# Optimization experiments

Hardware: AMD Instinct MI355X
Metric: run time of the kernel (lower is better)

Reference implementation:

```python
import jax, jax.numpy as jnp
import numpy as np

N_HEADS = 16
EPS = 1e-4


def setup_inputs() -> dict:
    key = jax.random.key(0)
    ks = jax.random.split(key, 9)
    B, L, E = 4, 4096, 1024
    s = 1.0 / np.sqrt(E)
    return {
        "x": jax.random.normal(ks[0], (B, L, E), dtype=jnp.float32),
        "Wq": jax.random.normal(ks[1], (E, E), dtype=jnp.float32) * s,
        "bq": jax.random.normal(ks[2], (E,), dtype=jnp.float32) * 0.01,
        "Wk": jax.random.normal(ks[3], (E, E), dtype=jnp.float32) * s,
        "bk": jax.random.normal(ks[4], (E,), dtype=jnp.float32) * 0.01,
        "Wv": jax.random.normal(ks[5], (E, E), dtype=jnp.float32) * s,
        "bv": jax.random.normal(ks[6], (E,), dtype=jnp.float32) * 0.01,
        "Wo": jax.random.normal(ks[7], (E, E), dtype=jnp.float32) * s,
        "bo": jax.random.normal(ks[8], (E,), dtype=jnp.float32) * 0.01,
    }


def _cosformer(x, Wq, bq, Wk, bk, Wv, bv, Wo, bo):
    B, L, E = x.shape
    H = N_HEADS
    hd = E // H
    # torch Linear: y = x @ W.T + b; self-attention so q=k=v source is x
    q = jax.nn.relu(jnp.einsum('ble,fe->blf', x, Wq) + bq)
    k = jax.nn.relu(jnp.einsum('ble,fe->blf', x, Wk) + bk)
    v = jnp.einsum('ble,fe->blf', x, Wv) + bv
    # (B, L, E) -> (B*H, L, hd)  [matches torch view(L, B*H, hd).transpose(0,1)]
    def split_heads(t):
        return t.reshape(B, L, H, hd).transpose(0, 2, 1, 3).reshape(B * H, L, hd)
    q, k, v = split_heads(q), split_heads(k), split_heads(v)
    m = L  # src_len == tgt_len
    idx = (np.pi / 2) * jnp.arange(1, m + 1, dtype=jnp.float32) / m  # (m,)
    sin = jnp.sin(idx)[None, :, None]
    cos = jnp.cos(idx)[None, :, None]
    q_ = jnp.concatenate([q * sin, q * cos], axis=-1)  # (BH, L, 2hd)
    k_ = jnp.concatenate([k * sin, k * cos], axis=-1)
    kv = jnp.einsum('nld,nlm->ndm', k_, v)             # (BH, 2hd, hd)
    z = 1.0 / jnp.maximum(jnp.einsum('nld,nd->nl', q_, k_.sum(axis=1)), EPS)
    attn = jnp.einsum('nld,ndm->nlm', q_, kv) * z[:, :, None]  # (BH, L, hd)
    # (B*H, L, hd) -> (B, L, E)
    out = attn.reshape(B, H, L, hd).transpose(0, 2, 1, 3).reshape(B, L, E)
    return jnp.einsum('ble,fe->blf', out, Wo) + bo


def reference(x, Wq, bq, Wk, bk, Wv, bv, Wo, bo):
    return _cosformer(x, Wq, bq, Wk, bk, Wv, bv, Wo, bo)
```

## Files before the change

### kernel.cpp

```cpp
#include <hip/hip_runtime.h>


typedef unsigned short u16;
typedef unsigned int u32;
typedef __attribute__((ext_vector_type(8))) __bf16 bf16x8;
typedef __attribute__((ext_vector_type(4))) float f32x4;

#define PI_HALF 1.57079632679489662f
#define EPS_Z 1e-4f

__device__ __forceinline__ u16 f32_to_bf16(float f) {
    union { float f; unsigned int u; } x; x.f = f;
    unsigned int lsb = (x.u >> 16) & 1u;
    x.u += 0x7fffu + lsb;
    return (u16)(x.u >> 16);
}
__device__ __forceinline__ float bf16_to_f32(u16 u) {
    union { float f; unsigned int u; } x; x.u = ((unsigned int)u) << 16;
    return x.f;
}

typedef __attribute__((address_space(1))) void amdgpu_global_t;
typedef __attribute__((address_space(3))) void amdgpu_lds_t;
__device__ __forceinline__ void async_load16(const u16* g, u16* l) {
    __builtin_amdgcn_global_load_lds((amdgpu_global_t*)g, (amdgpu_lds_t*)l, 16, 0, 0);
}

__global__ __launch_bounds__(256) void cvt_bf16(const float* __restrict__ in,
                                                u16* __restrict__ out, int n4) {
    int i = blockIdx.x * 256 + threadIdx.x;
    if (i >= n4) return;
    float4 f = ((const float4*)in)[i];
    ushort4 o;
    o.x = f32_to_bf16(f.x); o.y = f32_to_bf16(f.y);
    o.z = f32_to_bf16(f.z); o.w = f32_to_bf16(f.w);
    ((ushort4*)out)[i] = o;
}

__global__ __launch_bounds__(256) void cvt_w4(const float* __restrict__ w0,
                                              const float* __restrict__ w1,
                                              const float* __restrict__ w2,
                                              const float* __restrict__ w3,
                                              u16* __restrict__ wcat) {
    const float* src = (blockIdx.y == 0) ? w0 : (blockIdx.y == 1) ? w1
                     : (blockIdx.y == 2) ? w2 : w3;
    u16* dst = wcat + (size_t)blockIdx.y * 1048576;
    int i = blockIdx.x * 256 + threadIdx.x;
    float4 f = ((const float4*)src)[i];
    ushort4 o;
    o.x = f32_to_bf16(f.x); o.y = f32_to_bf16(f.y);
    o.z = f32_to_bf16(f.z); o.w = f32_to_bf16(f.w);
    ((ushort4*)dst)[i] = o;
}

__global__ __launch_bounds__(256) void gemm_qkv(const u16* __restrict__ A,
                                                const u16* __restrict__ Wcat,
                                                const float* __restrict__ bq,
                                                const float* __restrict__ bk,
                                                const float* __restrict__ bv,
                                                u16* __restrict__ qo,
                                                u16* __restrict__ ko,
                                                u16* __restrict__ vo) {
    __shared__ u16 As[128 * 32];
    __shared__ u16 Bs[128 * 32];
    const int K = 1024;
    const int tid  = threadIdx.x;
    const int wave = tid >> 6;
    const int lane = tid & 63;
    const int quad = lane >> 4;
    const int l15  = lane & 15;
    const long tileM = (long)blockIdx.x * 128;
    const long tileN = (long)blockIdx.y * 128;
    const int mat = blockIdx.y >> 3;
    const float* bias = (mat == 0) ? bq : (mat == 1) ? bk : bv;
    u16* outp = (mat == 0) ? qo : (mat == 1) ? ko : vo;
    const bool relu = (mat < 2);
    const int wm = (wave >> 1) * 64;
    const int wn = (wave & 1) * 64;
    const int s_row = wave * 32 + (lane >> 2);
    const int s_col = (lane & 3) * 8;

    const u16* gA = A    + (tileM + s_row) * (long)K + s_col;
    const u16* gB = Wcat + (tileN + s_row) * (long)K + s_col;
    u16* lA = &As[wave * 1024];
    u16* lB = &Bs[wave * 1024];

    f32x4 acc[4][4] = {};

    for (int kb = 0; kb < K; kb += 32) {
        async_load16(gA,                lA);
        async_load16(gA + 16 * (long)K, lA + 512);
        async_load16(gB,                lB);
        async_load16(gB + 16 * (long)K, lB + 512);
        gA += 32; gB += 32;
        __syncthreads();
        bf16x8 af[4], bf[4];
#pragma unroll
        for (int i = 0; i < 4; i++) {
            af[i] = *(const bf16x8*)&As[(wm + i * 16 + l15) * 32 + quad * 8];
            bf[i] = *(const bf16x8*)&Bs[(wn + i * 16 + l15) * 32 + quad * 8];
        }
#pragma unroll
        for (int i = 0; i < 4; i++)
#pragma unroll
            for (int j = 0; j < 4; j++)
                acc[i][j] = __builtin_amdgcn_mfma_f32_16x16x32_bf16(
                    af[i], bf[j], acc[i][j], 0, 0, 0);
        __syncthreads();
    }

#pragma unroll
    for (int j = 0; j < 4; j++) {
        const long n = tileN + wn + j * 16 + l15;
        const int nl = (int)n & 1023;
        const float bv_ = bias[nl];
#pragma unroll
        for (int i = 0; i < 4; i++) {
            const long m0 = tileM + wm + i * 16 + quad * 4;
#pragma unroll
            for (int r = 0; r < 4; r++) {
                float v = acc[i][j][r] + bv_;
                if (relu) v = fmaxf(v, 0.0f);
                outp[(m0 + r) * 1024 + nl] = f32_to_bf16(v);
            }
        }
    }
}

__global__ __launch_bounds__(256) void gemm_o(const u16* __restrict__ A,
                                              const u16* __restrict__ Bw,
                                              const float* __restrict__ bias,
                                              float* __restrict__ Cout,
                                              int M, int N, int K) {
    __shared__ u16 As[128 * 32];
    __shared__ u16 Bs[128 * 32];
    const int tid  = threadIdx.x;
    const int wave = tid >> 6;
    const int lane = tid & 63;
    const int quad = lane >> 4;
    const int l15  = lane & 15;
    const long tileM = (long)blockIdx.x * 128;
    const long tileN = (long)blockIdx.y * 128;
    const int wm = (wave >> 1) * 64;
    const int wn = (wave & 1) * 64;
    const int s_row = wave * 32 + (lane >> 2);
    const int s_col = (lane & 3) * 8;

    const u16* gA = A  + (tileM + s_row) * (long)K + s_col;
    const u16* gB = Bw + (tileN + s_row) * (long)K + s_col;
    u16* lA = &As[wave * 1024];
    u16* lB = &Bs[wave * 1024];

    f32x4 acc[4][4] = {};

    for (int kb = 0; kb < K; kb += 32) {
        async_load16(gA,                lA);
        async_load16(gA + 16 * (long)K, lA + 512);
        async_load16(gB,                lB);
        async_load16(gB + 16 * (long)K, lB + 512);
        gA += 32; gB += 32;
        __syncthreads();
        bf16x8 af[4], bf[4];
#pragma unroll
        for (int i = 0; i < 4; i++) {
            af[i] = *(const bf16x8*)&As[(wm + i * 16 + l15) * 32 + quad * 8];
            bf[i] = *(const bf16x8*)&Bs[(wn + i * 16 + l15) * 32 + quad * 8];
        }
#pragma unroll
        for (int i = 0; i < 4; i++)
#pragma unroll
            for (int j = 0; j < 4; j++)
                acc[i][j] = __builtin_amdgcn_mfma_f32_16x16x32_bf16(
                    af[i], bf[j], acc[i][j], 0, 0, 0);
        __syncthreads();
    }

#pragma unroll
    for (int j = 0; j < 4; j++) {
        const long n = tileN + wn + j * 16 + l15;
        const float bv = bias[n];
#pragma unroll
        for (int i = 0; i < 4; i++) {
            const long m0 = tileM + wm + i * 16 + quad * 4;
#pragma unroll
            for (int r = 0; r < 4; r++)
                Cout[(m0 + r) * (long)N + n] = acc[i][j][r] + bv;
        }
    }
}

__global__ __launch_bounds__(256) void kv_mfma(const u16* __restrict__ kmat,
                                               const u16* __restrict__ vmat,
                                               float* __restrict__ part) {
    __shared__ u16 Ak[64 * 40];
    __shared__ u16 Bv[64 * 40];
    const int tid = threadIdx.x;
    const int wave = tid >> 6, lane = tid & 63;
    const int quad = lane >> 4, l15 = lane & 15;
    const int head = blockIdx.y;
    const int b = head >> 4, h = head & 15;
    const int l0 = blockIdx.x * 512;
    const int sl = tid >> 3;
    const int sc8 = tid & 7;
    const int scol = sl ^ ((sc8 & 3) << 3);
    const int krow_base = (wave & 1) * 32;
    const bool use_cos = (wave >> 1) != 0;
    const int mbase = wave * 32;

    float sv[8], cv[8];
#pragma unroll
    for (int e = 0; e < 8; e++) {
        float ang = (PI_HALF / 4096.0f) * (float)(l0 + quad * 8 + e + 1);
        sv[e] = sinf(ang); cv[e] = cosf(ang);
    }
    const float cD = 0.9999247018391445f;
    const float sD = 0.0122715382857199f;

    bf16x8 onesf;
#pragma unroll
    for (int e = 0; e < 8; e++)
        onesf[e] = (l15 == 0) ? (__bf16)1.0f : (__bf16)0.0f;

    f32x4 acc[2][5] = {};

    for (int kt = 0; kt < 16; kt++) {
        const long row = ((long)b * 4096 + l0 + kt * 32 + sl) * 1024 + h * 64 + sc8 * 8;
        uint4 kk = *(const uint4*)(kmat + row);
        uint4 vv = *(const uint4*)(vmat + row);
        const u16* kp = (const u16*)&kk;
        const u16* vp = (const u16*)&vv;
#pragma unroll
        for (int e = 0; e < 8; e++) {
            const int d = sc8 * 8 + e;
            Ak[d * 40 + scol] = kp[e];
            Bv[d * 40 + scol] = vp[e];
        }
        __syncthreads();

        bf16x8 af[2];
#pragma unroll
        for (int i = 0; i < 2; i++) {
            const int d = krow_base + i * 16 + l15;
            const int q2 = (quad ^ ((d >> 3) & 3)) * 8;
            bf16x8 raw = *(const bf16x8*)&Ak[d * 40 + q2];
            bf16x8 sc;
#pragma unroll
            for (int e = 0; e < 8; e++)
                sc[e] = (__bf16)((float)raw[e] * (use_cos ? cv[e] : sv[e]));
            af[i] = sc;
        }
        bf16x8 bfr[5];
#pragma unroll
        for (int j = 0; j < 4; j++) {
            const int n = j * 16 + l15;
            const int q2 = (quad ^ ((n >> 3) & 3)) * 8;
            bfr[j] = *(const bf16x8*)&Bv[n * 40 + q2];
        }
        bfr[4] = onesf;
#pragma unroll
        for (int i = 0; i < 2; i++)
#pragma unroll
            for (int j = 0; j < 5; j++)
                acc[i][j] = __builtin_amdgcn_mfma_f32_16x16x32_bf16(
                    af[i], bfr[j], acc[i][j], 0, 0, 0);

#pragma unroll
        for (int e = 0; e < 8; e++) {
            const float ns = sv[e] * cD + cv[e] * sD;
            cv[e] = cv[e] * cD - sv[e] * sD;
            sv[e] = ns;
        }
        __syncthreads();
    }

    float* op = part + ((long)blockIdx.x * 64 + head) * 10240;
#pragma unroll
    for (int i = 0; i < 2; i++)
#pragma unroll
        for (int j = 0; j < 5; j++)
#pragma unroll
            for (int r = 0; r < 4; r++)
                op[(mbase + i * 16 + quad * 4 + r) * 80 + j * 16 + l15] = acc[i][j][r];
}

__global__ __launch_bounds__(256) void kv_reduce_t(const float* __restrict__ part,
                                                   u16* __restrict__ Bt) {
    __shared__ float accs[32 * 81];
    const int head = blockIdx.y, d2t = blockIdx.x;
    const float* bp = part + (long)head * 10240 + d2t * 32 * 80;
    for (int idx = threadIdx.x; idx < 2560; idx += 256) {
        float s = 0.0f;
#pragma unroll
        for (int c = 0; c < 8; c++) s += bp[(long)c * 655360 + idx];
        const int d2 = idx / 80, n = idx - d2 * 80;
        accs[d2 * 81 + n] = s;
    }
    __syncthreads();
    for (int idx = threadIdx.x; idx < 2560; idx += 256) {
        const int n = idx >> 5, d2 = idx & 31;
        Bt[(long)head * 10240 + n * 128 + d2t * 32 + d2] = f32_to_bf16(accs[d2 * 81 + n]);
    }
}

__global__ __launch_bounds__(256) void attn_mfma(const u16* __restrict__ qb,
                                                 const u16* __restrict__ Bt,
                                                 u16* __restrict__ merged) {
    __shared__ __align__(16) u16 As[128 * 72];
    __shared__ __align__(16) u16 Bs[80 * 136];
    const int tid = threadIdx.x;
    const int wave = tid >> 6, lane = tid & 63;
    const int quad = lane >> 4, l15 = lane & 15;
    const int head = blockIdx.y;
    const int b = head >> 4, h = head & 15;
    const int tm = blockIdx.x * 128;
    const long b4 = (long)b * 4096;

    for (int c = tid; c < 1024; c += 256) {
        const int row = c >> 3, c8 = c & 7;
        uint4 t = *(const uint4*)(qb + (b4 + tm + row) * 1024 + h * 64 + c8 * 8);
        *(uint4*)&As[row * 72 + c8 * 8] = t;
    }
    for (int c = tid; c < 1280; c += 256) {
        const int row = c >> 4, c16 = c & 15;
        uint4 t = *(const uint4*)(Bt + (long)head * 10240 + row * 128 + c16 * 8);
        *(uint4*)&Bs[row * 136 + c16 * 8] = t;
    }
    const int wm = wave * 32;
    float snl[2], csl[2];
#pragma unroll
    for (int i = 0; i < 2; i++) {
        const int l = tm + wm + i * 16 + l15;
        const float idx = PI_HALF * (float)(l + 1) * (1.0f / 4096.0f);
        snl[i] = sinf(idx); csl[i] = cosf(idx);
    }
    __syncthreads();

    f32x4 acc[2][5] = {};
#pragma unroll
    for (int kb = 0; kb < 4; kb++) {
        const int qc = (kb & 1) * 32 + quad * 8;
        bf16x8 af[2];
#pragma unroll
        for (int i = 0; i < 2; i++) {
            bf16x8 raw = *(const bf16x8*)&As[(wm + i * 16 + l15) * 72 + qc];
            const float s = (kb < 2) ? snl[i] : csl[i];
            bf16x8 sc;
#pragma unroll
            for (int e = 0; e < 8; e++) sc[e] = (__bf16)((float)raw[e] * s);
            af[i] = sc;
        }
        bf16x8 bf[5];
#pragma unroll
        for (int j = 0; j < 5; j++)
            bf[j] = *(const bf16x8*)&Bs[(j * 16 + l15) * 136 + kb * 32 + quad * 8];
#pragma unroll
        for (int i = 0; i < 2; i++)
#pragma unroll
            for (int j = 0; j < 5; j++)
                acc[i][j] = __builtin_amdgcn_mfma_f32_16x16x32_bf16(
                    af[i], bf[j], acc[i][j], 0, 0, 0);
    }

#pragma unroll
    for (int i = 0; i < 2; i++) {
        float z[4];
#pragma unroll
        for (int r = 0; r < 4; r++) {
            const float den = __shfl(acc[i][4][r], lane & 0x30, 64);
            z[r] = 1.0f / fmaxf(den, EPS_Z);
        }
#pragma unroll
        for (int j = 0; j < 4; j++)
#pragma unroll
            for (int r = 0; r < 4; r++) {
                const int l = tm + wm + i * 16 + quad * 4 + r;
                merged[(b4 + l) * 1024 + h * 64 + j * 16 + l15] =
                    f32_to_bf16(acc[i][j][r] * z[r]);
            }
    }
}

extern "C" void kernel_launch(void* const* d_in, const int* in_sizes, int n_in,
                              void* d_out, int out_size, void* d_ws, size_t ws_size,
                              hipStream_t stream) {
    (void)in_sizes; (void)n_in; (void)out_size; (void)ws_size;
    const float* x  = (const float*)d_in[0];
    const float* Wq = (const float*)d_in[1];
    const float* bq = (const float*)d_in[2];
    const float* Wk = (const float*)d_in[3];
    const float* bk = (const float*)d_in[4];
    const float* Wv = (const float*)d_in[5];
    const float* bv = (const float*)d_in[6];
    const float* Wo = (const float*)d_in[7];
    const float* bo = (const float*)d_in[8];
    float* out = (float*)d_out;

    const int M = 16384, E = 1024;
    char* ws = (char*)d_ws;
    const size_t MB = 1048576;
    u16* xb   = (u16*)(ws);
    u16* qb   = (u16*)(ws + 32 * MB);
    u16* kb   = (u16*)(ws + 64 * MB);
    u16* vb   = (u16*)(ws + 96 * MB);
    u16* wcat = (u16*)(ws + 128 * MB);
    u16* wob  = wcat + 3 * (size_t)E * E;
    u16* Btb  = (u16*)(ws + 136 * MB);
    float* part = (float*)xb;
    u16* mergedb = kb;

    cvt_bf16<<<dim3(M * E / 4 / 256), dim3(256), 0, stream>>>(x, xb, M * E / 4);
    cvt_w4<<<dim3(E * E / 4 / 256, 4), dim3(256), 0, stream>>>(Wq, Wk, Wv, Wo, wcat);

    gemm_qkv<<<dim3(M / 128, 24), dim3(256), 0, stream>>>(xb, wcat, bq, bk, bv,
                                                          qb, kb, vb);

    kv_mfma<<<dim3(8, 64), dim3(256), 0, stream>>>(kb, vb, part);
    kv_reduce_t<<<dim3(4, 64), dim3(256), 0, stream>>>(part, Btb);
    attn_mfma<<<dim3(32, 64), dim3(256), 0, stream>>>(qb, Btb, mergedb);

    gemm_o<<<dim3(M / 128, E / 128), dim3(256), 0, stream>>>(mergedb, wob, bo,
                                                             out, M, E, E);
}
```

Baseline: 384.0 us.

## Write K and V transposed from QKV GEMM so kv_mfma reads fragments directly

```diff
diff --git a/kernel.cpp b/kernel.cpp
--- a/kernel.cpp
+++ b/kernel.cpp
@@ -59,8 +59,8 @@
                                                 const float* __restrict__ bk,
                                                 const float* __restrict__ bv,
                                                 u16* __restrict__ qo,
-                                                u16* __restrict__ ko,
-                                                u16* __restrict__ vo) {
+                                                u16* __restrict__ kTo,
+                                                u16* __restrict__ vTo) {
     __shared__ u16 As[128 * 32];
     __shared__ u16 Bs[128 * 32];
     const int K = 1024;
@@ -73,8 +73,6 @@
     const long tileN = (long)blockIdx.y * 128;
     const int mat = blockIdx.y >> 3;
     const float* bias = (mat == 0) ? bq : (mat == 1) ? bk : bv;
-    u16* outp = (mat == 0) ? qo : (mat == 1) ? ko : vo;
-    const bool relu = (mat < 2);
     const int wm = (wave >> 1) * 64;
     const int wn = (wave & 1) * 64;
     const int s_row = wave * 32 + (lane >> 2);
@@ -109,19 +107,43 @@
         __syncthreads();
     }
 
-#pragma unroll
-    for (int j = 0; j < 4; j++) {
-        const long n = tileN + wn + j * 16 + l15;
-        const int nl = (int)n & 1023;
-        const float bv_ = bias[nl];
-#pragma unroll
-        for (int i = 0; i < 4; i++) {
-            const long m0 = tileM + wm + i * 16 + quad * 4;
-#pragma unroll
-            for (int r = 0; r < 4; r++) {
-                float v = acc[i][j][r] + bv_;
-                if (relu) v = fmaxf(v, 0.0f);
-                outp[(m0 + r) * 1024 + nl] = f32_to_bf16(v);
+    if (mat == 0) {
+#pragma unroll
+        for (int j = 0; j < 4; j++) {
+            const int nl = (int)(tileN + wn + j * 16 + l15) & 1023;
+            const float bv_ = bias[nl];
+#pragma unroll
+            for (int i = 0; i < 4; i++) {
+                const long m0 = tileM + wm + i * 16 + quad * 4;
+#pragma unroll
+                for (int r = 0; r < 4; r++) {
+                    float v = fmaxf(acc[i][j][r] + bv_, 0.0f);
+                    qo[(m0 + r) * 1024 + nl] = f32_to_bf16(v);
+                }
+            }
+        }
+    } else {
+        u16* outT = (mat == 1) ? kTo : vTo;
+        const bool relu = (mat == 1);
+#pragma unroll
+        for (int j = 0; j < 4; j++) {
+            const int nl = (int)(tileN + wn + j * 16 + l15) & 1023;
+            const float bv_ = bias[nl];
+#pragma unroll
+            for (int i = 0; i < 4; i++) {
+                const long m0 = tileM + wm + i * 16 + quad * 4;
+                float v0 = acc[i][j][0] + bv_;
+                float v1 = acc[i][j][1] + bv_;
+                float v2 = acc[i][j][2] + bv_;
+                float v3 = acc[i][j][3] + bv_;
+                if (relu) {
+                    v0 = fmaxf(v0, 0.0f); v1 = fmaxf(v1, 0.0f);
+                    v2 = fmaxf(v2, 0.0f); v3 = fmaxf(v3, 0.0f);
+                }
+                u32 p0 = (u32)f32_to_bf16(v0) | ((u32)f32_to_bf16(v1) << 16);
+                u32 p1 = (u32)f32_to_bf16(v2) | ((u32)f32_to_bf16(v3) << 16);
+                u32* dst = (u32*)(outT + (size_t)nl * 16384 + m0);
+                dst[0] = p0; dst[1] = p1;
             }
         }
     }
@@ -189,28 +211,35 @@
     }
 }
 
-__global__ __launch_bounds__(256) void kv_mfma(const u16* __restrict__ kmat,
-                                               const u16* __restrict__ vmat,
-                                               float* __restrict__ part) {
-    __shared__ u16 Ak[64 * 40];
-    __shared__ u16 Bv[64 * 40];
+__global__ __launch_bounds__(256) void kv_mfma(const u16* __restrict__ kT,
+                                               const u16* __restrict__ vT,
+                                               u16* __restrict__ part) {
     const int tid = threadIdx.x;
     const int wave = tid >> 6, lane = tid & 63;
     const int quad = lane >> 4, l15 = lane & 15;
     const int head = blockIdx.y;
     const int b = head >> 4, h = head & 15;
-    const int l0 = blockIdx.x * 512;
-    const int sl = tid >> 3;
-    const int sc8 = tid & 7;
-    const int scol = sl ^ ((sc8 & 3) << 3);
-    const int krow_base = (wave & 1) * 32;
+    const long col0 = (long)b * 4096 + blockIdx.x * 256 + quad * 8;
     const bool use_cos = (wave >> 1) != 0;
     const int mbase = wave * 32;
 
+    const u16* ka[2];
+#pragma unroll
+    for (int i = 0; i < 2; i++) {
+        const int d = (mbase + i * 16 + l15) & 63;
+        ka[i] = kT + (size_t)(h * 64 + d) * 16384 + col0;
+    }
+    const u16* va[4];
+#pragma unroll
+    for (int j = 0; j < 4; j++) {
+        const int n = j * 16 + l15;
+        va[j] = vT + (size_t)(h * 64 + n) * 16384 + col0;
+    }
+
     float sv[8], cv[8];
 #pragma unroll
     for (int e = 0; e < 8; e++) {
-        float ang = (PI_HALF / 4096.0f) * (float)(l0 + quad * 8 + e + 1);
+        float ang = (PI_HALF / 4096.0f) * (float)(blockIdx.x * 256 + quad * 8 + e + 1);
         sv[e] = sinf(ang); cv[e] = cosf(ang);
     }
     const float cD = 0.9999247018391445f;
@@ -223,82 +252,62 @@
 
     f32x4 acc[2][5] = {};
 
-    for (int kt = 0; kt < 16; kt++) {
-        const long row = ((long)b * 4096 + l0 + kt * 32 + sl) * 1024 + h * 64 + sc8 * 8;
-        uint4 kk = *(const uint4*)(kmat + row);
-        uint4 vv = *(const uint4*)(vmat + row);
-        const u16* kp = (const u16*)&kk;
-        const u16* vp = (const u16*)&vv;
-#pragma unroll
-        for (int e = 0; e < 8; e++) {
-            const int d = sc8 * 8 + e;
-            Ak[d * 40 + scol] = kp[e];
-            Bv[d * 40 + scol] = vp[e];
-        }
-        __syncthreads();
-
+    for (int kt = 0; kt < 8; kt++) {
+        bf16x8 kraw[2], bfr[5];
+#pragma unroll
+        for (int i = 0; i < 2; i++) kraw[i] = *(const bf16x8*)(ka[i] + kt * 32);
+#pragma unroll
+        for (int j = 0; j < 4; j++) bfr[j] = *(const bf16x8*)(va[j] + kt * 32);
+        bfr[4] = onesf;
         bf16x8 af[2];
 #pragma unroll
-        for (int i = 0; i < 2; i++) {
-            const int d = krow_base + i * 16 + l15;
-            const int q2 = (quad ^ ((d >> 3) & 3)) * 8;
-            bf16x8 raw = *(const bf16x8*)&Ak[d * 40 + q2];
-            bf16x8 sc;
+        for (int i = 0; i < 2; i++)
 #pragma unroll
             for (int e = 0; e < 8; e++)
-                sc[e] = (__bf16)((float)raw[e] * (use_cos ? cv[e] : sv[e]));
-            af[i] = sc;
-        }
-        bf16x8 bfr[5];
-#pragma unroll
-        for (int j = 0; j < 4; j++) {
-            const int n = j * 16 + l15;
-            const int q2 = (quad ^ ((n >> 3) & 3)) * 8;
-            bfr[j] = *(const bf16x8*)&Bv[n * 40 + q2];
-        }
-        bfr[4] = onesf;
+                af[i][e] = (__bf16)((float)kraw[i][e] * (use_cos ? cv[e] : sv[e]));
 #pragma unroll
         for (int i = 0; i < 2; i++)
 #pragma unroll
             for (int j = 0; j < 5; j++)
                 acc[i][j] = __builtin_amdgcn_mfma_f32_16x16x32_bf16(
                     af[i], bfr[j], acc[i][j], 0, 0, 0);
-
 #pragma unroll
         for (int e = 0; e < 8; e++) {
             const float ns = sv[e] * cD + cv[e] * sD;
             cv[e] = cv[e] * cD - sv[e] * sD;
             sv[e] = ns;
         }
-        __syncthreads();
-    }
-
-    float* op = part + ((long)blockIdx.x * 64 + head) * 10240;
+    }
+
+    u16* op = part + ((size_t)blockIdx.x * 64 + head) * 10240;
 #pragma unroll
     for (int i = 0; i < 2; i++)
 #pragma unroll
         for (int j = 0; j < 5; j++)
 #pragma unroll
             for (int r = 0; r < 4; r++)
-                op[(mbase + i * 16 + quad * 4 + r) * 80 + j * 16 + l15] = acc[i][j][r];
-}
-
-__global__ __launch_bounds__(256) void kv_reduce_t(const float* __restrict__ part,
+                op[(mbase + i * 16 + quad * 4 + r) * 80 + j * 16 + l15] =
+                    f32_to_bf16(acc[i][j][r]);
+}
+
+__global__ __launch_bounds__(256) void kv_reduce_t(const u16* __restrict__ part,
                                                    u16* __restrict__ Bt) {
     __shared__ float accs[32 * 81];
     const int head = blockIdx.y, d2t = blockIdx.x;
-    const float* bp = part + (long)head * 10240 + d2t * 32 * 80;
+    const u16* bp = part + (size_t)head * 10240 + d2t * 32 * 80;
     for (int idx = threadIdx.x; idx < 2560; idx += 256) {
         float s = 0.0f;
 #pragma unroll
-        for (int c = 0; c < 8; c++) s += bp[(long)c * 655360 + idx];
+        for (int c = 0; c < 16; c++)
+            s += bf16_to_f32(bp[(size_t)c * 655360 + idx]);
         const int d2 = idx / 80, n = idx - d2 * 80;
         accs[d2 * 81 + n] = s;
     }
     __syncthreads();
     for (int idx = threadIdx.x; idx < 2560; idx += 256) {
         const int n = idx >> 5, d2 = idx & 31;
-        Bt[(long)head * 10240 + n * 128 + d2t * 32 + d2] = f32_to_bf16(accs[d2 * 81 + n]);
+        Bt[(size_t)head * 10240 + n * 128 + d2t * 32 + d2] =
+            f32_to_bf16(accs[d2 * 81 + n]);
     }
 }
 
@@ -400,22 +409,22 @@
     const size_t MB = 1048576;
     u16* xb   = (u16*)(ws);
     u16* qb   = (u16*)(ws + 32 * MB);
-    u16* kb   = (u16*)(ws + 64 * MB);
-    u16* vb   = (u16*)(ws + 96 * MB);
+    u16* kTb  = (u16*)(ws + 64 * MB);
+    u16* vTb  = (u16*)(ws + 96 * MB);
     u16* wcat = (u16*)(ws + 128 * MB);
     u16* wob  = wcat + 3 * (size_t)E * E;
     u16* Btb  = (u16*)(ws + 136 * MB);
-    float* part = (float*)xb;
-    u16* mergedb = kb;
+    u16* partb = xb;
+    u16* mergedb = kTb;
 
     cvt_bf16<<<dim3(M * E / 4 / 256), dim3(256), 0, stream>>>(x, xb, M * E / 4);
     cvt_w4<<<dim3(E * E / 4 / 256, 4), dim3(256), 0, stream>>>(Wq, Wk, Wv, Wo, wcat);
 
     gemm_qkv<<<dim3(M / 128, 24), dim3(256), 0, stream>>>(xb, wcat, bq, bk, bv,
-                                                          qb, kb, vb);
-
-    kv_mfma<<<dim3(8, 64), dim3(256), 0, stream>>>(kb, vb, part);
-    kv_reduce_t<<<dim3(4, 64), dim3(256), 0, stream>>>(part, Btb);
+                                                          qb, kTb, vTb);
+
+    kv_mfma<<<dim3(16, 64), dim3(256), 0, stream>>>(kTb, vTb, partb);
+    kv_reduce_t<<<dim3(4, 64), dim3(256), 0, stream>>>(partb, Btb);
     attn_mfma<<<dim3(32, 64), dim3(256), 0, stream>>>(qb, Btb, mergedb);
 
     gemm_o<<<dim3(M / 128, E / 128), dim3(256), 0, stream>>>(mergedb, wob, bo,
```

Result: slower. 413.5 us (+7.7%).
